# Kernel optimization log

Hardware: AMD Instinct MI355X
Metric: run time of the kernel (lower is better)

## Reference

```python
import jax, jax.numpy as jnp
import numpy as np

B, T, E, H, D_PRICE = 16, 2048, 128, 4, 512


def setup_inputs() -> dict:
    key = jax.random.key(0)
    ks = jax.random.split(key, 22)
    f32 = jnp.float32

    def w(k, shape):
        fan_in = shape[0]
        return (jax.random.normal(k, shape, f32) / np.sqrt(fan_in)).astype(f32)

    def b(k, n):
        return (jax.random.normal(k, (n,), f32) * 0.01).astype(f32)

    inp = {
        # OHLC prices, positive, normalized scale
        "ohlc": jax.random.uniform(ks[0], (B, T, 4), f32, 0.5, 1.5),
        # ohlc_proj: Linear(4, 64)
        "Wp": w(ks[1], (4, 64)), "bp": b(ks[2], 64),
        # curvature_net: Linear(64,128) -> ReLU -> Linear(128,32)
        "Wc1": w(ks[3], (64, 128)), "bc1": b(ks[4], 128),
        "Wc2": w(ks[5], (128, 32)), "bc2": b(ks[6], 32),
        # volatility_net: Linear(64,64) -> ReLU -> Linear(64,16)
        "Wv1": w(ks[7], (64, 64)), "bv1": b(ks[8], 64),
        "Wv2": w(ks[9], (64, 16)), "bv2": b(ks[10], 16),
        # sr_field_net: Linear(64,64) -> ReLU -> Linear(64,16)
        "Ws1": w(ks[11], (64, 64)), "bs1": b(ks[12], 64),
        "Ws2": w(ks[13], (64, 16)), "bs2": b(ks[14], 16),
        # MultiheadAttention(embed_dim=128, num_heads=4): fused in-proj + out-proj
        "Wqkv": w(ks[15], (E, 3 * E)), "bqkv": b(ks[16], 3 * E),
        "Wo": w(ks[17], (E, E)), "bo": b(ks[18], E),
        # output_proj: Linear(128, d_price)
        "Wout": w(ks[19], (E, D_PRICE)), "bout": b(ks[20], D_PRICE),
    }
    return inp


def _mlp(x, W1, b1, W2, b2):
    return jax.nn.relu(x @ W1 + b1) @ W2 + b2


def reference(ohlc, Wp, bp, Wc1, bc1, Wc2, bc2, Wv1, bv1, Wv2, bv2,
              Ws1, bs1, Ws2, bs2, Wqkv, bqkv, Wo, bo, Wout, bout):
    # NB: compute_curvature / compute_volatility_surface / detect_sr_levels
    # in the original forward are dead code (results never used), so they are
    # omitted here; output math is identical.
    e = ohlc @ Wp + bp                                   # [B,T,64]
    feats = jnp.concatenate([
        e,
        _mlp(e, Wc1, bc1, Wc2, bc2),                     # [B,T,32]
        _mlp(e, Wv1, bv1, Wv2, bv2),                     # [B,T,16]
        _mlp(e, Ws1, bs1, Ws2, bs2),                     # [B,T,16]
    ], axis=-1)                                          # [B,T,128]

    Bn, Tn, En = feats.shape
    dh = En // H
    qkv = feats @ Wqkv + bqkv                            # [B,T,3E]
    q, k, v = jnp.split(qkv, 3, axis=-1)

    def heads(x):
        return x.reshape(Bn, Tn, H, dh).transpose(0, 2, 1, 3)  # [B,H,T,dh]

    q, k, v = heads(q), heads(k), heads(v)
    scores = jnp.einsum('bhqd,bhkd->bhqk', q, k) / np.sqrt(dh).astype(feats.dtype)
    a = jax.nn.softmax(scores, axis=-1)                  # [B,H,T,T]
    o = jnp.einsum('bhqk,bhkd->bhqd', a, v)
    o = o.transpose(0, 2, 1, 3).reshape(Bn, Tn, En)
    attended = o @ Wo + bo                               # [B,T,128]

    pooled = attended.mean(axis=1)                       # [B,128]
    return pooled @ Wout + bout                          # [B,512]
```

## Files before the change

### kernel.cpp

```cpp
#include <hip/hip_runtime.h>


typedef __attribute__((ext_vector_type(4)))  float f32x4;
typedef __attribute__((ext_vector_type(16))) float f32x16;
typedef __attribute__((ext_vector_type(4)))  short short4v;
typedef __attribute__((ext_vector_type(8)))  short short8v;

static __device__ __forceinline__ unsigned short f2b(float f) {
    unsigned int u = __builtin_bit_cast(unsigned int, f);
    u += 0x7fffu + ((u >> 16) & 1u);
    return (unsigned short)(u >> 16);
}

static __device__ __forceinline__ unsigned int cvtpk_bf16(float a, float b) {
    unsigned int r;
    asm volatile("v_cvt_pk_bf16_f32 %0, %1, %2" : "=v"(r) : "v"(a), "v"(b));
    return r;
}

__global__ __launch_bounds__(256) void prep_kernel(
    const float* Wc1, const float* Wc2, const float* Wv1, const float* Wv2,
    const float* Ws1, const float* Ws2,
    unsigned short* wc1t, unsigned short* wc2t, unsigned short* wv1t,
    unsigned short* wv2t, unsigned short* ws1t, unsigned short* ws2t,
    float* pooled, float* qkmax)
{
    int idx = blockIdx.x * 256 + threadIdx.x;
    if (idx < 8192)  { int n = idx >> 6, kk = idx & 63;  wc1t[idx] = f2b(Wc1[kk*128 + n]); return; }
    idx -= 8192;
    if (idx < 4096)  { int n = idx >> 7, kk = idx & 127; wc2t[idx] = f2b(Wc2[kk*32  + n]); return; }
    idx -= 4096;
    if (idx < 4096)  { int n = idx >> 6, kk = idx & 63;  wv1t[idx] = f2b(Wv1[kk*64  + n]); return; }
    idx -= 4096;
    if (idx < 1024)  { int n = idx >> 6, kk = idx & 63;  wv2t[idx] = f2b(Wv2[kk*16  + n]); return; }
    idx -= 1024;
    if (idx < 4096)  { int n = idx >> 6, kk = idx & 63;  ws1t[idx] = f2b(Ws1[kk*64  + n]); return; }
    idx -= 4096;
    if (idx < 1024)  { int n = idx >> 6, kk = idx & 63;  ws2t[idx] = f2b(Ws2[kk*16  + n]); return; }
    idx -= 1024;
    if (idx < 2048)  { pooled[idx] = 0.f; return; }
    idx -= 2048;
    if (idx < 128)   qkmax[idx] = 0.f;
}

__global__ __launch_bounds__(256) void wqkv_trans(
    const float* __restrict__ W, unsigned short* __restrict__ outT)
{
    __shared__ float tile[32][33];
    int bidn = blockIdx.x % 12, bidk = blockIdx.x / 12;
    int n0 = bidn * 32, k0 = bidk * 32;
    int tid = threadIdx.x;
    {
        int r = tid >> 3, cq = tid & 7;
        float4 v = *(const float4*)(W + (size_t)(k0 + r) * 384 + n0 + cq * 4);
        tile[r][cq*4+0] = v.x; tile[r][cq*4+1] = v.y;
        tile[r][cq*4+2] = v.z; tile[r][cq*4+3] = v.w;
    }
    __syncthreads();
    {
        int nr = tid >> 3, kq = tid & 7;
        union { unsigned short us[4]; short4v v; } pk;
#pragma unroll
        for (int j = 0; j < 4; ++j) pk.us[j] = f2b(tile[kq*4+j][nr]);
        *(short4v*)(outT + (size_t)(n0 + nr) * 128 + k0 + kq * 4) = pk.v;
    }
}

template<int N, int K, int A_ROWB, bool RELU, bool TO_LDS>
static __device__ __forceinline__ void tile_gemm(
    const char* As, const unsigned short* __restrict__ BT,
    const float* __restrict__ bias, char* Ht,
    unsigned short* __restrict__ gOut, int ocol,
    int m0, int w, int lane)
{
    constexpr int ASL = A_ROWB / 16, NT = N / 16, KS = K / 32;
    int l15 = lane & 15, hi4 = lane >> 4;
    f32x4 acc[NT];
#pragma unroll
    for (int nt = 0; nt < NT; ++nt)
#pragma unroll
        for (int r = 0; r < 4; ++r) acc[nt][r] = 0.f;

#pragma unroll
    for (int ks = 0; ks < KS; ++ks) {
        int slot = ks * 4 + hi4;
        int m = w * 16 + l15;
        short8v af = *(const short8v*)(As + m * A_ROWB + ((slot ^ (m & (ASL - 1))) << 4));
#pragma unroll
        for (int nt = 0; nt < NT; ++nt) {
            int n = nt * 16 + l15;
            short8v bf = *(const short8v*)(BT + (size_t)n * K + slot * 8);
            acc[nt] = __builtin_amdgcn_mfma_f32_16x16x32_bf16(af, bf, acc[nt], 0, 0, 0);
        }
    }
#pragma unroll
    for (int nt = 0; nt < NT; ++nt) {
        int n = nt * 16 + l15;
        float bv = bias[n];
#pragma unroll
        for (int r = 0; r < 4; ++r) {
            int m = w * 16 + hi4 * 4 + r;
            float v = acc[nt][r] + bv;
            if (RELU) v = fmaxf(v, 0.f);
            if (TO_LDS) {
                *(unsigned short*)(Ht + m * 256 + ((((n >> 3) ^ (m & 15))) << 4) + (n & 7) * 2) = f2b(v);
            } else {
                gOut[(size_t)(m0 + m) * 128 + ocol + n] = f2b(v);
            }
        }
    }
}

__global__ __launch_bounds__(256) void fused_mlp(
    const float* __restrict__ ohlc, const float* __restrict__ Wp, const float* __restrict__ bp,
    const unsigned short* __restrict__ wc1t, const float* __restrict__ bc1,
    const unsigned short* __restrict__ wc2t, const float* __restrict__ bc2,
    const unsigned short* __restrict__ wv1t, const float* __restrict__ bv1,
    const unsigned short* __restrict__ wv2t, const float* __restrict__ bv2,
    const unsigned short* __restrict__ ws1t, const float* __restrict__ bs1,
    const unsigned short* __restrict__ ws2t, const float* __restrict__ bs2,
    unsigned short* __restrict__ feats)
{
    __shared__ float wp[256];
    __shared__ float bpl[64];
    __shared__ char Et[64 * 128];
    __shared__ char Ht[64 * 256];

    int tid = threadIdx.x;
    int m0 = blockIdx.x * 64;
    wp[tid] = Wp[tid];
    if (tid < 64) bpl[tid] = bp[tid];
    __syncthreads();

    {
        int tok = tid >> 2, jq = tid & 3;
        float4 ov = ((const float4*)ohlc)[m0 + tok];
#pragma unroll
        for (int c = 0; c < 2; ++c) {
            int sl = jq * 2 + c;
            union { unsigned short us[8]; short8v v; } pk;
#pragma unroll
            for (int jj = 0; jj < 8; ++jj) {
                int j = sl * 8 + jj;
                float e = bpl[j] + ov.x * wp[j] + ov.y * wp[64 + j]
                                 + ov.z * wp[128 + j] + ov.w * wp[192 + j];
                pk.us[jj] = f2b(e);
            }
            *(short8v*)(Et + tok * 128 + ((sl ^ (tok & 7)) << 4)) = pk.v;
            *(short8v*)(feats + (size_t)(m0 + tok) * 128 + sl * 8) = pk.v;
        }
    }
    __syncthreads();

    int lane = tid & 63, w = tid >> 6;
    tile_gemm<128, 64, 128, true,  true >(Et, wc1t, bc1, Ht, feats, 0,   m0, w, lane);
    tile_gemm<32, 128, 256, false, false>(Ht, wc2t, bc2, Ht, feats, 64,  m0, w, lane);
    tile_gemm<64,  64, 128, true,  true >(Et, wv1t, bv1, Ht, feats, 0,   m0, w, lane);
    tile_gemm<16,  64, 256, false, false>(Ht, wv2t, bv2, Ht, feats, 96,  m0, w, lane);
    tile_gemm<64,  64, 128, true,  true >(Et, ws1t, bs1, Ht, feats, 0,   m0, w, lane);
    tile_gemm<16,  64, 256, false, false>(Ht, ws2t, bs2, Ht, feats, 112, m0, w, lane);
}

__global__ __launch_bounds__(256) void qkv_gemm(
    const unsigned short* __restrict__ feats,
    const unsigned short* __restrict__ wqkvt, const float* __restrict__ bqkv,
    unsigned short* __restrict__ qg, unsigned short* __restrict__ kg,
    unsigned short* __restrict__ vTg, float* __restrict__ qkmax)
{
    constexpr int ROWB = 256, CPR = 16;
    __shared__ short8v smemv[4096];
    char* As = (char*)smemv;
    char* Bs = (char*)smemv + 32768;

    int tid = threadIdx.x;
    int m0 = blockIdx.x * 128;
    int sel = blockIdx.y;
    const unsigned short* BT = wqkvt + (size_t)sel * 128 * 128;

    for (int c = tid; c < 128 * CPR; c += 256) {
        int m = c / CPR, s = c % CPR;
        short8v v = *(const short8v*)(feats + (size_t)(m0 + m) * 128 + s * 8);
        *(short8v*)(As + m * ROWB + ((s ^ (m & 15)) * 16)) = v;
    }
    for (int c = tid; c < 128 * CPR; c += 256) {
        int n = c / CPR, s = c % CPR;
        short8v v = *(const short8v*)(BT + (size_t)n * 128 + s * 8);
        *(short8v*)(Bs + n * ROWB + ((s ^ (n & 15)) * 16)) = v;
    }
    __syncthreads();

    int lane = tid & 63, w = tid >> 6;
    int l15 = lane & 15, hi4 = lane >> 4;

    f32x4 acc[2][8];
#pragma unroll
    for (int mt = 0; mt < 2; ++mt)
#pragma unroll
        for (int nt = 0; nt < 8; ++nt)
#pragma unroll
            for (int r = 0; r < 4; ++r) acc[mt][nt][r] = 0.f;

#pragma unroll
    for (int ks = 0; ks < 4; ++ks) {
        int slot = ks * 4 + hi4;
        short8v af[2];
#pragma unroll
        for (int mt = 0; mt < 2; ++mt) {
            int m = w * 32 + mt * 16 + l15;
            af[mt] = *(const short8v*)(As + m * ROWB + ((slot ^ (m & 15)) * 16));
        }
#pragma unroll
        for (int nt = 0; nt < 8; ++nt) {
            int n = nt * 16 + l15;
            short8v bf = *(const short8v*)(Bs + n * ROWB + ((slot ^ (n & 15)) * 16));
            acc[0][nt] = __builtin_amdgcn_mfma_f32_16x16x32_bf16(af[0], bf, acc[0][nt], 0, 0, 0);
            acc[1][nt] = __builtin_amdgcn_mfma_f32_16x16x32_bf16(af[1], bf, acc[1][nt], 0, 0, 0);
        }
    }

    const float QSCALE = 1.4426950408889634f * 0.17677669529663687f;
    int b = m0 >> 11, tp0 = m0 & 2047;

    if (sel == 2) {
#pragma unroll
        for (int mt = 0; mt < 2; ++mt)
#pragma unroll
            for (int nt = 0; nt < 8; ++nt) {
                int n = nt * 16 + l15;
                float bv = bqkv[256 + n];
                int h = n >> 5, dh = n & 31;
                float v0 = acc[mt][nt][0] + bv, v1 = acc[mt][nt][1] + bv;
                float v2 = acc[mt][nt][2] + bv, v3 = acc[mt][nt][3] + bv;
                uint2 pk;
                pk.x = cvtpk_bf16(v0, v1);
                pk.y = cvtpk_bf16(v2, v3);
                int t = tp0 + w * 32 + mt * 16 + hi4 * 4;
                *(uint2*)(vTg + ((size_t)(b * 4 + h) * 32 + dh) * 2048 + t) = pk;
            }
    } else {
        float amax[4] = {0.f, 0.f, 0.f, 0.f};
        float scale = (sel == 0) ? QSCALE : 1.0f;
#pragma unroll
        for (int mt = 0; mt < 2; ++mt)
#pragma unroll
            for (int nt = 0; nt < 8; ++nt) {
                int n = nt * 16 + l15;
                float bv = bqkv[sel * 128 + n];
#pragma unroll
                for (int r = 0; r < 4; ++r) {
                    float v = (acc[mt][nt][r] + bv) * scale;
                    amax[nt >> 1] = fmaxf(amax[nt >> 1], fabsf(v));
                    int m = w * 32 + mt * 16 + hi4 * 4 + r;
                    *(unsigned short*)(As + m * 256 + (((n >> 3) ^ (m & 7)) << 4) + (n & 7) * 2) = f2b(v);
                }
            }
#pragma unroll
        for (int g = 0; g < 4; ++g) {
            float mv = amax[g];
            mv = fmaxf(mv, __shfl_xor(mv, 1));  mv = fmaxf(mv, __shfl_xor(mv, 2));
            mv = fmaxf(mv, __shfl_xor(mv, 4));  mv = fmaxf(mv, __shfl_xor(mv, 8));
            mv = fmaxf(mv, __shfl_xor(mv, 16)); mv = fmaxf(mv, __shfl_xor(mv, 32));
            if (lane == 0)
                atomicMax((int*)(qkmax + sel * 64 + b * 4 + g), __float_as_int(mv));
        }
        __syncthreads();
        unsigned short* og = (sel == 0) ? qg : kg;
#pragma unroll
        for (int it = 0; it < 8; ++it) {
            int ch = it * 256 + tid;
            int m = ch >> 4, c = ch & 15;
            short8v vv = *(const short8v*)(As + m * 256 + ((c ^ (m & 7)) << 4));
            int h = c >> 2, dq = c & 3;
            *(short8v*)(og + ((size_t)(b * 4 + h) * 2048 + tp0 + m) * 32 + dq * 8) = vv;
        }
    }
}

__global__ __launch_bounds__(256) void attn_kernel(
    const unsigned short* __restrict__ qg, const unsigned short* __restrict__ kg,
    const unsigned short* __restrict__ vTg, const float* __restrict__ qkmax,
    float* __restrict__ pooled)
{
    __shared__ short8v VsBuf[4 * 256];
    char* Vs = (char*)VsBuf;

    int tid = threadIdx.x, bid = blockIdx.x;
    int bh = bid & 63, qb = bid >> 6;
    int b = bh >> 2;
    int lane = tid & 63, w = tid >> 6;
    int l31 = lane & 31, hi = lane >> 5;
    int q0 = qb * 128 + w * 32;

    const unsigned short* qrow = qg + ((size_t)bh * 2048 + q0 + l31) * 32;
    short8v Qf0 = *(const short8v*)(qrow + hi * 8);
    short8v Qf1 = *(const short8v*)(qrow + 16 + hi * 8);

    float negM0 = -(32.0f * qkmax[bh] * qkmax[64 + bh]);

    f32x16 accO;
#pragma unroll
    for (int r = 0; r < 16; ++r) accO[r] = 0.f;
    float lsum = 0.f;

    const char* kp = (const char*)(kg + (size_t)bh * 2048 * 32) + (size_t)l31 * 64 + hi * 16;
    int vdh = w * 8 + (lane >> 3);
    const char* vp = (const char*)(vTg + ((size_t)bh * 32 + vdh) * 2048) +
                     (((lane & 7) ^ (vdh & 7)) << 4);
    int vdst = (w * 64 + lane) * 16;

    auto step = [&](int t, short8v (&kC)[4], short8v& vC,
                    short8v (&kN)[4], short8v& vN, char* bufp) {
        if (t < 31) {
            const char* p = kp + (size_t)(t + 1) * 4096;
            kN[0] = *(const short8v*)(p);
            kN[1] = *(const short8v*)(p + 32);
            kN[2] = *(const short8v*)(p + 2048);
            kN[3] = *(const short8v*)(p + 2080);
            vN = *(const short8v*)(vp + (size_t)(t + 1) * 128);
        }
        *(short8v*)(bufp + vdst) = vC;
        asm volatile("s_waitcnt lgkmcnt(0)" ::: "memory");
        __builtin_amdgcn_s_barrier();
        asm volatile("" ::: "memory");
#pragma unroll
        for (int sub = 0; sub < 2; ++sub) {
            f32x16 s;
#pragma unroll
            for (int r = 0; r < 16; ++r) s[r] = negM0;
            s = __builtin_amdgcn_mfma_f32_32x32x16_bf16(kC[sub * 2 + 0], Qf0, s, 0, 0, 0);
            s = __builtin_amdgcn_mfma_f32_32x32x16_bf16(kC[sub * 2 + 1], Qf1, s, 0, 0, 0);
            float p_[16];
            float ps = 0.f;
#pragma unroll
            for (int r = 0; r < 16; ++r) {
                p_[r] = __builtin_amdgcn_exp2f(s[r]);
                ps += p_[r];
            }
            lsum += ps;
#pragma unroll
            for (int c2 = 0; c2 < 2; ++c2) {
                unsigned int wa = cvtpk_bf16(p_[c2 * 8 + 0], p_[c2 * 8 + 1]);
                unsigned int wb = cvtpk_bf16(p_[c2 * 8 + 2], p_[c2 * 8 + 3]);
                unsigned int wc = cvtpk_bf16(p_[c2 * 8 + 4], p_[c2 * 8 + 5]);
                unsigned int wd = cvtpk_bf16(p_[c2 * 8 + 6], p_[c2 * 8 + 7]);
                asm volatile("v_permlane32_swap_b32 %0, %1" : "+v"(wa), "+v"(wc));
                asm volatile("v_permlane32_swap_b32 %0, %1" : "+v"(wb), "+v"(wd));
                union { unsigned int u[4]; short8v v; } pf;
                pf.u[0] = wa; pf.u[1] = wb; pf.u[2] = wc; pf.u[3] = wd;

                short8v vf = *(const short8v*)(bufp + l31 * 128 +
                              (((sub * 4 + c2 * 2 + hi) ^ (l31 & 7)) << 4));
                accO = __builtin_amdgcn_mfma_f32_32x32x16_bf16(vf, pf.v, accO, 0, 0, 0);
            }
        }
    };

    short8v kE[4], kO[4], vE, vO;
    {
        kE[0] = *(const short8v*)(kp);
        kE[1] = *(const short8v*)(kp + 32);
        kE[2] = *(const short8v*)(kp + 2048);
        kE[3] = *(const short8v*)(kp + 2080);
        vE = *(const short8v*)(vp);
    }
#pragma unroll 1
    for (int g = 0; g < 8; ++g) {
        int t0 = g * 4;
        step(t0 + 0, kE, vE, kO, vO, Vs + 0 * 4096);
        step(t0 + 1, kO, vO, kE, vE, Vs + 1 * 4096);
        step(t0 + 2, kE, vE, kO, vO, Vs + 2 * 4096);
        step(t0 + 3, kO, vO, kE, vE, Vs + 3 * 4096);
    }

    lsum += __shfl_xor(lsum, 32);
    float inv = 1.0f / lsum;
#pragma unroll
    for (int r = 0; r < 16; ++r) {
        float v = accO[r] * inv;
        v += __shfl_xor(v, 1); v += __shfl_xor(v, 2); v += __shfl_xor(v, 4);
        v += __shfl_xor(v, 8); v += __shfl_xor(v, 16);
        if (l31 == 0) {
            int dh = (r & 3) + 8 * (r >> 2) + 4 * hi;
            atomicAdd(pooled + b * 128 + (bh & 3) * 32 + dh, v);
        }
    }
}

__global__ __launch_bounds__(256) void head_kernel(
    const float* __restrict__ pooled, const float* __restrict__ Wo,
    const float* __restrict__ bo, const float* __restrict__ Wout,
    const float* __restrict__ bout, float* __restrict__ out)
{
    int bq = blockIdx.x, tid = threadIdx.x;
    __shared__ float pl[128], mid[128];
    if (tid < 128) pl[tid] = pooled[bq * 128 + tid] * (1.f / 2048.f);
    __syncthreads();
    if (tid < 128) {
        float s = bo[tid];
#pragma unroll 4
        for (int c = 0; c < 128; ++c) s += pl[c] * Wo[c * 128 + tid];
        mid[tid] = s;
    }
    __syncthreads();
    for (int j = tid; j < 512; j += 256) {
        float s = bout[j];
#pragma unroll 4
        for (int i = 0; i < 128; ++i) s += mid[i] * Wout[i * 512 + j];
        out[bq * 512 + j] = s;
    }
}

extern "C" void kernel_launch(void* const* d_in, const int* in_sizes, int n_in,
                              void* d_out, int out_size, void* d_ws, size_t ws_size,
                              hipStream_t stream) {
    (void)in_sizes; (void)n_in; (void)out_size; (void)ws_size;
    const float* ohlc = (const float*)d_in[0];
    const float* Wp   = (const float*)d_in[1];  const float* bp   = (const float*)d_in[2];
    const float* Wc1  = (const float*)d_in[3];  const float* bc1  = (const float*)d_in[4];
    const float* Wc2  = (const float*)d_in[5];  const float* bc2  = (const float*)d_in[6];
    const float* Wv1  = (const float*)d_in[7];  const float* bv1  = (const float*)d_in[8];
    const float* Wv2  = (const float*)d_in[9];  const float* bv2  = (const float*)d_in[10];
    const float* Ws1  = (const float*)d_in[11]; const float* bs1  = (const float*)d_in[12];
    const float* Ws2  = (const float*)d_in[13]; const float* bs2  = (const float*)d_in[14];
    const float* Wqkv = (const float*)d_in[15]; const float* bqkv = (const float*)d_in[16];
    const float* Wo   = (const float*)d_in[17]; const float* bo   = (const float*)d_in[18];
    const float* Wout = (const float*)d_in[19]; const float* bout = (const float*)d_in[20];
    float* out = (float*)d_out;
    char* ws = (char*)d_ws;

    const size_t MB8 = 8388608;
    unsigned short* feats = (unsigned short*)(ws);
    unsigned short* qg    = (unsigned short*)(ws + 1 * MB8);
    unsigned short* kg    = (unsigned short*)(ws + 2 * MB8);
    unsigned short* vTg   = (unsigned short*)(ws + 3 * MB8);
    float*          pooled = (float*)(ws + 4 * MB8);
    float*          qkmax  = (float*)(ws + 4 * MB8 + 8192);
    unsigned short* wc1t  = (unsigned short*)(ws + 4 * MB8 + 8192 + 512);
    unsigned short* wc2t  = wc1t + 8192;
    unsigned short* wv1t  = wc2t + 4096;
    unsigned short* wv2t  = wv1t + 4096;
    unsigned short* ws1t  = wv2t + 1024;
    unsigned short* ws2t  = ws1t + 4096;
    unsigned short* wqkvt = ws2t + 1024;

    prep_kernel<<<97, 256, 0, stream>>>(Wc1, Wc2, Wv1, Wv2, Ws1, Ws2,
                                        wc1t, wc2t, wv1t, wv2t, ws1t, ws2t,
                                        pooled, qkmax);
    wqkv_trans<<<48, 256, 0, stream>>>(Wqkv, wqkvt);
    fused_mlp<<<512, 256, 0, stream>>>(ohlc, Wp, bp, wc1t, bc1, wc2t, bc2,
                                       wv1t, bv1, wv2t, bv2, ws1t, bs1, ws2t, bs2, feats);
    qkv_gemm<<<dim3(256, 3), 256, 0, stream>>>(feats, wqkvt, bqkv, qg, kg, vTg, qkmax);
    attn_kernel<<<1024, 256, 0, stream>>>(qg, kg, vTg, qkmax, pooled);
    head_kernel<<<16, 256, 0, stream>>>(pooled, Wo, bo, Wout, bout, out);
}
```

Measured before the change: 155.1 us.

## Fuse MLP and QKV projection into one kernel, compute softmax row sums via MFMA

Merges the MLP feature kernel and the QKV GEMM into a single mega_kernel that keeps the 128-wide feature tile in LDS instead of writing it to global memory and reading it back. The Wqkv transpose is folded into prep_kernel, removing two launches. In attention, the softmax denominator is now accumulated with an extra MFMA against a ones vector rather than scalar adds plus a shuffle, and the score MMA starts from a precomputed NEGM accumulator. s_setprio is raised around the compute phase. The risk is that the fused kernel reads weights per wave from global memory without LDS staging, has smaller M tiles for QKV, and adds MFMA work in the attention inner loop.

```diff
diff --git a/kernel.cpp b/kernel.cpp
--- a/kernel.cpp
+++ b/kernel.cpp
@@ -19,13 +19,34 @@
 }
 
 __global__ __launch_bounds__(256) void prep_kernel(
-    const float* Wc1, const float* Wc2, const float* Wv1, const float* Wv2,
-    const float* Ws1, const float* Ws2,
-    unsigned short* wc1t, unsigned short* wc2t, unsigned short* wv1t,
-    unsigned short* wv2t, unsigned short* ws1t, unsigned short* ws2t,
-    float* pooled, float* qkmax)
-{
-    int idx = blockIdx.x * 256 + threadIdx.x;
+    const float* Wqkv, const float* Wc1, const float* Wc2, const float* Wv1,
+    const float* Wv2, const float* Ws1, const float* Ws2,
+    unsigned short* wqkvt, unsigned short* wc1t, unsigned short* wc2t,
+    unsigned short* wv1t, unsigned short* wv2t, unsigned short* ws1t,
+    unsigned short* ws2t, float* pooled, float* qkmax)
+{
+    int tid = threadIdx.x;
+    if (blockIdx.x < 48) {
+        __shared__ float tile[32][33];
+        int bidn = blockIdx.x % 12, bidk = blockIdx.x / 12;
+        int n0 = bidn * 32, k0 = bidk * 32;
+        {
+            int r = tid >> 3, cq = tid & 7;
+            float4 v = *(const float4*)(Wqkv + (size_t)(k0 + r) * 384 + n0 + cq * 4);
+            tile[r][cq*4+0] = v.x; tile[r][cq*4+1] = v.y;
+            tile[r][cq*4+2] = v.z; tile[r][cq*4+3] = v.w;
+        }
+        __syncthreads();
+        {
+            int nr = tid >> 3, kq = tid & 7;
+            union { unsigned short us[4]; short4v v; } pk;
+#pragma unroll
+            for (int j = 0; j < 4; ++j) pk.us[j] = f2b(tile[kq*4+j][nr]);
+            *(short4v*)(wqkvt + (size_t)(n0 + nr) * 128 + k0 + kq * 4) = pk.v;
+        }
+        return;
+    }
+    int idx = (blockIdx.x - 48) * 256 + tid;
     if (idx < 8192)  { int n = idx >> 6, kk = idx & 63;  wc1t[idx] = f2b(Wc1[kk*128 + n]); return; }
     idx -= 8192;
     if (idx < 4096)  { int n = idx >> 7, kk = idx & 127; wc2t[idx] = f2b(Wc2[kk*32  + n]); return; }
@@ -43,75 +64,91 @@
     if (idx < 128)   qkmax[idx] = 0.f;
 }
 
-__global__ __launch_bounds__(256) void wqkv_trans(
-    const float* __restrict__ W, unsigned short* __restrict__ outT)
-{
-    __shared__ float tile[32][33];
-    int bidn = blockIdx.x % 12, bidk = blockIdx.x / 12;
-    int n0 = bidn * 32, k0 = bidk * 32;
-    int tid = threadIdx.x;
-    {
-        int r = tid >> 3, cq = tid & 7;
-        float4 v = *(const float4*)(W + (size_t)(k0 + r) * 384 + n0 + cq * 4);
-        tile[r][cq*4+0] = v.x; tile[r][cq*4+1] = v.y;
-        tile[r][cq*4+2] = v.z; tile[r][cq*4+3] = v.w;
-    }
-    __syncthreads();
-    {
-        int nr = tid >> 3, kq = tid & 7;
-        union { unsigned short us[4]; short4v v; } pk;
-#pragma unroll
-        for (int j = 0; j < 4; ++j) pk.us[j] = f2b(tile[kq*4+j][nr]);
-        *(short4v*)(outT + (size_t)(n0 + nr) * 128 + k0 + kq * 4) = pk.v;
-    }
-}
-
-template<int N, int K, int A_ROWB, bool RELU, bool TO_LDS>
-static __device__ __forceinline__ void tile_gemm(
+template<int N, int K>
+static __device__ __forceinline__ void wave_gemm(
     const char* As, const unsigned short* __restrict__ BT,
-    const float* __restrict__ bias, char* Ht,
-    unsigned short* __restrict__ gOut, int ocol,
-    int m0, int w, int lane)
-{
-    constexpr int ASL = A_ROWB / 16, NT = N / 16, KS = K / 32;
+    int w, int lane, f32x4 (&acc)[N / 16])
+{
     int l15 = lane & 15, hi4 = lane >> 4;
-    f32x4 acc[NT];
-#pragma unroll
-    for (int nt = 0; nt < NT; ++nt)
+#pragma unroll
+    for (int nt = 0; nt < N / 16; ++nt)
 #pragma unroll
         for (int r = 0; r < 4; ++r) acc[nt][r] = 0.f;
-
-#pragma unroll
-    for (int ks = 0; ks < KS; ++ks) {
+#pragma unroll
+    for (int ks = 0; ks < K / 32; ++ks) {
         int slot = ks * 4 + hi4;
         int m = w * 16 + l15;
-        short8v af = *(const short8v*)(As + m * A_ROWB + ((slot ^ (m & (ASL - 1))) << 4));
-#pragma unroll
-        for (int nt = 0; nt < NT; ++nt) {
+        short8v af = *(const short8v*)(As + m * 256 + ((slot ^ (m & 15)) << 4));
+#pragma unroll
+        for (int nt = 0; nt < N / 16; ++nt) {
             int n = nt * 16 + l15;
             short8v bf = *(const short8v*)(BT + (size_t)n * K + slot * 8);
             acc[nt] = __builtin_amdgcn_mfma_f32_16x16x32_bf16(af, bf, acc[nt], 0, 0, 0);
         }
     }
-#pragma unroll
-    for (int nt = 0; nt < NT; ++nt) {
+}
+
+template<int N, bool RELU>
+static __device__ __forceinline__ void epi_lds(
+    f32x4 (&acc)[N / 16], const float* __restrict__ bias, int boff,
+    char* dst, int ocol, int w, int lane)
+{
+    int l15 = lane & 15, hi4 = lane >> 4;
+#pragma unroll
+    for (int nt = 0; nt < N / 16; ++nt) {
         int n = nt * 16 + l15;
-        float bv = bias[n];
+        float bv = bias[boff + n];
 #pragma unroll
         for (int r = 0; r < 4; ++r) {
             int m = w * 16 + hi4 * 4 + r;
             float v = acc[nt][r] + bv;
             if (RELU) v = fmaxf(v, 0.f);
-            if (TO_LDS) {
-                *(unsigned short*)(Ht + m * 256 + ((((n >> 3) ^ (m & 15))) << 4) + (n & 7) * 2) = f2b(v);
-            } else {
-                gOut[(size_t)(m0 + m) * 128 + ocol + n] = f2b(v);
-            }
-        }
-    }
-}
-
-__global__ __launch_bounds__(256) void fused_mlp(
+            int col = ocol + n;
+            *(unsigned short*)(dst + m * 256 + (((col >> 3) ^ (m & 15)) << 4) + (col & 7) * 2) = f2b(v);
+        }
+    }
+}
+
+static __device__ __forceinline__ void epi_qk(
+    f32x4 (&acc)[8], const float* __restrict__ bias, int boff, float scale,
+    unsigned short* __restrict__ og, float* qkmaxp,
+    int b, int tp0, int w, int lane, char* bounce)
+{
+    int l15 = lane & 15, hi4 = lane >> 4;
+    float amax[4] = {0.f, 0.f, 0.f, 0.f};
+#pragma unroll
+    for (int nt = 0; nt < 8; ++nt) {
+        int n = nt * 16 + l15;
+        float bv = bias[boff + n];
+#pragma unroll
+        for (int r = 0; r < 4; ++r) {
+            int m = w * 16 + hi4 * 4 + r;
+            float v = (acc[nt][r] + bv) * scale;
+            amax[nt >> 1] = fmaxf(amax[nt >> 1], fabsf(v));
+            *(unsigned short*)(bounce + m * 256 + (((n >> 3) ^ (m & 15)) << 4) + (n & 7) * 2) = f2b(v);
+        }
+    }
+#pragma unroll
+    for (int g = 0; g < 4; ++g) {
+        float mv = amax[g];
+        mv = fmaxf(mv, __shfl_xor(mv, 1));  mv = fmaxf(mv, __shfl_xor(mv, 2));
+        mv = fmaxf(mv, __shfl_xor(mv, 4));  mv = fmaxf(mv, __shfl_xor(mv, 8));
+        mv = fmaxf(mv, __shfl_xor(mv, 16)); mv = fmaxf(mv, __shfl_xor(mv, 32));
+        if (lane == 0)
+            atomicMax((int*)(qkmaxp + b * 4 + g), __float_as_int(mv));
+    }
+#pragma unroll
+    for (int it = 0; it < 4; ++it) {
+        int ch = it * 64 + lane;
+        int ml = ch >> 4, c = ch & 15;
+        int m = w * 16 + ml;
+        short8v vv = *(const short8v*)(bounce + m * 256 + ((c ^ (m & 15)) << 4));
+        int h = c >> 2, dq = c & 3;
+        *(short8v*)(og + ((size_t)(b * 4 + h) * 2048 + tp0 + m) * 32 + dq * 8) = vv;
+    }
+}
+
+__global__ __launch_bounds__(256) void mega_kernel(
     const float* __restrict__ ohlc, const float* __restrict__ Wp, const float* __restrict__ bp,
     const unsigned short* __restrict__ wc1t, const float* __restrict__ bc1,
     const unsigned short* __restrict__ wc2t, const float* __restrict__ bc2,
@@ -119,11 +156,13 @@
     const unsigned short* __restrict__ wv2t, const float* __restrict__ bv2,
     const unsigned short* __restrict__ ws1t, const float* __restrict__ bs1,
     const unsigned short* __restrict__ ws2t, const float* __restrict__ bs2,
-    unsigned short* __restrict__ feats)
+    const unsigned short* __restrict__ wqkvt, const float* __restrict__ bqkv,
+    unsigned short* __restrict__ qg, unsigned short* __restrict__ kg,
+    unsigned short* __restrict__ vTg, float* __restrict__ qkmax)
 {
     __shared__ float wp[256];
     __shared__ float bpl[64];
-    __shared__ char Et[64 * 128];
+    __shared__ char Ft[64 * 256];
     __shared__ char Ht[64 * 256];
 
     int tid = threadIdx.x;
@@ -146,132 +185,68 @@
                                  + ov.z * wp[128 + j] + ov.w * wp[192 + j];
                 pk.us[jj] = f2b(e);
             }
-            *(short8v*)(Et + tok * 128 + ((sl ^ (tok & 7)) << 4)) = pk.v;
-            *(short8v*)(feats + (size_t)(m0 + tok) * 128 + sl * 8) = pk.v;
-        }
-    }
-    __syncthreads();
+            *(short8v*)(Ft + tok * 256 + ((sl ^ (tok & 15)) << 4)) = pk.v;
+        }
+    }
 
     int lane = tid & 63, w = tid >> 6;
-    tile_gemm<128, 64, 128, true,  true >(Et, wc1t, bc1, Ht, feats, 0,   m0, w, lane);
-    tile_gemm<32, 128, 256, false, false>(Ht, wc2t, bc2, Ht, feats, 64,  m0, w, lane);
-    tile_gemm<64,  64, 128, true,  true >(Et, wv1t, bv1, Ht, feats, 0,   m0, w, lane);
-    tile_gemm<16,  64, 256, false, false>(Ht, wv2t, bv2, Ht, feats, 96,  m0, w, lane);
-    tile_gemm<64,  64, 128, true,  true >(Et, ws1t, bs1, Ht, feats, 0,   m0, w, lane);
-    tile_gemm<16,  64, 256, false, false>(Ht, ws2t, bs2, Ht, feats, 112, m0, w, lane);
-}
-
-__global__ __launch_bounds__(256) void qkv_gemm(
-    const unsigned short* __restrict__ feats,
-    const unsigned short* __restrict__ wqkvt, const float* __restrict__ bqkv,
-    unsigned short* __restrict__ qg, unsigned short* __restrict__ kg,
-    unsigned short* __restrict__ vTg, float* __restrict__ qkmax)
-{
-    constexpr int ROWB = 256, CPR = 16;
-    __shared__ short8v smemv[4096];
-    char* As = (char*)smemv;
-    char* Bs = (char*)smemv + 32768;
-
-    int tid = threadIdx.x;
-    int m0 = blockIdx.x * 128;
-    int sel = blockIdx.y;
-    const unsigned short* BT = wqkvt + (size_t)sel * 128 * 128;
-
-    for (int c = tid; c < 128 * CPR; c += 256) {
-        int m = c / CPR, s = c % CPR;
-        short8v v = *(const short8v*)(feats + (size_t)(m0 + m) * 128 + s * 8);
-        *(short8v*)(As + m * ROWB + ((s ^ (m & 15)) * 16)) = v;
-    }
-    for (int c = tid; c < 128 * CPR; c += 256) {
-        int n = c / CPR, s = c % CPR;
-        short8v v = *(const short8v*)(BT + (size_t)n * 128 + s * 8);
-        *(short8v*)(Bs + n * ROWB + ((s ^ (n & 15)) * 16)) = v;
-    }
-    __syncthreads();
-
-    int lane = tid & 63, w = tid >> 6;
-    int l15 = lane & 15, hi4 = lane >> 4;
-
-    f32x4 acc[2][8];
-#pragma unroll
-    for (int mt = 0; mt < 2; ++mt)
-#pragma unroll
-        for (int nt = 0; nt < 8; ++nt)
-#pragma unroll
-            for (int r = 0; r < 4; ++r) acc[mt][nt][r] = 0.f;
-
-#pragma unroll
-    for (int ks = 0; ks < 4; ++ks) {
-        int slot = ks * 4 + hi4;
-        short8v af[2];
-#pragma unroll
-        for (int mt = 0; mt < 2; ++mt) {
-            int m = w * 32 + mt * 16 + l15;
-            af[mt] = *(const short8v*)(As + m * ROWB + ((slot ^ (m & 15)) * 16));
-        }
+    {
+        f32x4 a8[8];
+        wave_gemm<128, 64>(Ft, wc1t, w, lane, a8);
+        epi_lds<128, true>(a8, bc1, 0, Ht, 0, w, lane);
+    }
+    {
+        f32x4 a2[2];
+        wave_gemm<32, 128>(Ht, wc2t, w, lane, a2);
+        epi_lds<32, false>(a2, bc2, 0, Ft, 64, w, lane);
+    }
+    {
+        f32x4 a4[4];
+        wave_gemm<64, 64>(Ft, wv1t, w, lane, a4);
+        epi_lds<64, true>(a4, bv1, 0, Ht, 0, w, lane);
+    }
+    {
+        f32x4 a1[1];
+        wave_gemm<16, 64>(Ht, wv2t, w, lane, a1);
+        epi_lds<16, false>(a1, bv2, 0, Ft, 96, w, lane);
+    }
+    {
+        f32x4 a4[4];
+        wave_gemm<64, 64>(Ft, ws1t, w, lane, a4);
+        epi_lds<64, true>(a4, bs1, 0, Ht, 0, w, lane);
+    }
+    {
+        f32x4 a1[1];
+        wave_gemm<16, 64>(Ht, ws2t, w, lane, a1);
+        epi_lds<16, false>(a1, bs2, 0, Ft, 112, w, lane);
+    }
+
+    const float QSCALE = 1.4426950408889634f * 0.17677669529663687f;
+    int b = m0 >> 11, tp0 = m0 & 2047;
+    {
+        f32x4 aq[8];
+        wave_gemm<128, 128>(Ft, wqkvt, w, lane, aq);
+        epi_qk(aq, bqkv, 0, QSCALE, qg, qkmax, b, tp0, w, lane, Ht);
+    }
+    {
+        f32x4 ak[8];
+        wave_gemm<128, 128>(Ft, wqkvt + 128 * 128, w, lane, ak);
+        epi_qk(ak, bqkv, 128, 1.0f, kg, qkmax + 64, b, tp0, w, lane, Ht);
+    }
+    {
+        f32x4 av[8];
+        wave_gemm<128, 128>(Ft, wqkvt + 2 * 128 * 128, w, lane, av);
+        int l15 = lane & 15, hi4 = lane >> 4;
 #pragma unroll
         for (int nt = 0; nt < 8; ++nt) {
             int n = nt * 16 + l15;
-            short8v bf = *(const short8v*)(Bs + n * ROWB + ((slot ^ (n & 15)) * 16));
-            acc[0][nt] = __builtin_amdgcn_mfma_f32_16x16x32_bf16(af[0], bf, acc[0][nt], 0, 0, 0);
-            acc[1][nt] = __builtin_amdgcn_mfma_f32_16x16x32_bf16(af[1], bf, acc[1][nt], 0, 0, 0);
-        }
-    }
-
-    const float QSCALE = 1.4426950408889634f * 0.17677669529663687f;
-    int b = m0 >> 11, tp0 = m0 & 2047;
-
-    if (sel == 2) {
-#pragma unroll
-        for (int mt = 0; mt < 2; ++mt)
-#pragma unroll
-            for (int nt = 0; nt < 8; ++nt) {
-                int n = nt * 16 + l15;
-                float bv = bqkv[256 + n];
-                int h = n >> 5, dh = n & 31;
-                float v0 = acc[mt][nt][0] + bv, v1 = acc[mt][nt][1] + bv;
-                float v2 = acc[mt][nt][2] + bv, v3 = acc[mt][nt][3] + bv;
-                uint2 pk;
-                pk.x = cvtpk_bf16(v0, v1);
-                pk.y = cvtpk_bf16(v2, v3);
-                int t = tp0 + w * 32 + mt * 16 + hi4 * 4;
-                *(uint2*)(vTg + ((size_t)(b * 4 + h) * 32 + dh) * 2048 + t) = pk;
-            }
-    } else {
-        float amax[4] = {0.f, 0.f, 0.f, 0.f};
-        float scale = (sel == 0) ? QSCALE : 1.0f;
-#pragma unroll
-        for (int mt = 0; mt < 2; ++mt)
-#pragma unroll
-            for (int nt = 0; nt < 8; ++nt) {
-                int n = nt * 16 + l15;
-                float bv = bqkv[sel * 128 + n];
-#pragma unroll
-                for (int r = 0; r < 4; ++r) {
-                    float v = (acc[mt][nt][r] + bv) * scale;
-                    amax[nt >> 1] = fmaxf(amax[nt >> 1], fabsf(v));
-                    int m = w * 32 + mt * 16 + hi4 * 4 + r;
-                    *(unsigned short*)(As + m * 256 + (((n >> 3) ^ (m & 7)) << 4) + (n & 7) * 2) = f2b(v);
-                }
-            }
-#pragma unroll
-        for (int g = 0; g < 4; ++g) {
-            float mv = amax[g];
-            mv = fmaxf(mv, __shfl_xor(mv, 1));  mv = fmaxf(mv, __shfl_xor(mv, 2));
-            mv = fmaxf(mv, __shfl_xor(mv, 4));  mv = fmaxf(mv, __shfl_xor(mv, 8));
-            mv = fmaxf(mv, __shfl_xor(mv, 16)); mv = fmaxf(mv, __shfl_xor(mv, 32));
-            if (lane == 0)
-                atomicMax((int*)(qkmax + sel * 64 + b * 4 + g), __float_as_int(mv));
-        }
-        __syncthreads();
-        unsigned short* og = (sel == 0) ? qg : kg;
-#pragma unroll
-        for (int it = 0; it < 8; ++it) {
-            int ch = it * 256 + tid;
-            int m = ch >> 4, c = ch & 15;
-            short8v vv = *(const short8v*)(As + m * 256 + ((c ^ (m & 7)) << 4));
-            int h = c >> 2, dq = c & 3;
-            *(short8v*)(og + ((size_t)(b * 4 + h) * 2048 + tp0 + m) * 32 + dq * 8) = vv;
+            float bv = bqkv[256 + n];
+            int h = n >> 5, dh = n & 31;
+            uint2 pk;
+            pk.x = cvtpk_bf16(av[nt][0] + bv, av[nt][1] + bv);
+            pk.y = cvtpk_bf16(av[nt][2] + bv, av[nt][3] + bv);
+            int t = tp0 + w * 16 + hi4 * 4;
+            *(uint2*)(vTg + ((size_t)(b * 4 + h) * 32 + dh) * 2048 + t) = pk;
         }
     }
 }
@@ -296,17 +271,31 @@
     short8v Qf1 = *(const short8v*)(qrow + 16 + hi * 8);
 
     float negM0 = -(32.0f * qkmax[bh] * qkmax[64 + bh]);
-
-    f32x16 accO;
-#pragma unroll
-    for (int r = 0; r < 16; ++r) accO[r] = 0.f;
-    float lsum = 0.f;
+    f32x16 NEGM;
+#pragma unroll
+    for (int r = 0; r < 16; ++r) NEGM[r] = negM0;
+
+    f32x16 accO, lacc;
+#pragma unroll
+    for (int r = 0; r < 16; ++r) { accO[r] = 0.f; lacc[r] = 0.f; }
+
+    short8v ONES;
+    {
+        union { unsigned short us[8]; short8v v; } u;
+#pragma unroll
+        for (int j = 0; j < 8; ++j) u.us[j] = 0x3F80;
+        ONES = u.v;
+    }
 
     const char* kp = (const char*)(kg + (size_t)bh * 2048 * 32) + (size_t)l31 * 64 + hi * 16;
     int vdh = w * 8 + (lane >> 3);
     const char* vp = (const char*)(vTg + ((size_t)bh * 32 + vdh) * 2048) +
                      (((lane & 7) ^ (vdh & 7)) << 4);
     int vdst = (w * 64 + lane) * 16;
+    int voff[4];
+#pragma unroll
+    for (int j = 0; j < 4; ++j)
+        voff[j] = l31 * 128 + (((2 * j + hi) ^ (l31 & 7)) << 4);
 
     auto step = [&](int t, short8v (&kC)[4], short8v& vC,
                     short8v (&kN)[4], short8v& vN, char* bufp) {
@@ -322,21 +311,14 @@
         asm volatile("s_waitcnt lgkmcnt(0)" ::: "memory");
         __builtin_amdgcn_s_barrier();
         asm volatile("" ::: "memory");
+        __builtin_amdgcn_s_setprio(1);
 #pragma unroll
         for (int sub = 0; sub < 2; ++sub) {
-            f32x16 s;
-#pragma unroll
-            for (int r = 0; r < 16; ++r) s[r] = negM0;
-            s = __builtin_amdgcn_mfma_f32_32x32x16_bf16(kC[sub * 2 + 0], Qf0, s, 0, 0, 0);
+            f32x16 s = __builtin_amdgcn_mfma_f32_32x32x16_bf16(kC[sub * 2 + 0], Qf0, NEGM, 0, 0, 0);
             s = __builtin_amdgcn_mfma_f32_32x32x16_bf16(kC[sub * 2 + 1], Qf1, s, 0, 0, 0);
             float p_[16];
-            float ps = 0.f;
-#pragma unroll
-            for (int r = 0; r < 16; ++r) {
-                p_[r] = __builtin_amdgcn_exp2f(s[r]);
-                ps += p_[r];
-            }
-            lsum += ps;
+#pragma unroll
+            for (int r = 0; r < 16; ++r) p_[r] = __builtin_amdgcn_exp2f(s[r]);
 #pragma unroll
             for (int c2 = 0; c2 < 2; ++c2) {
                 unsigned int wa = cvtpk_bf16(p_[c2 * 8 + 0], p_[c2 * 8 + 1]);
@@ -348,11 +330,12 @@
                 union { unsigned int u[4]; short8v v; } pf;
                 pf.u[0] = wa; pf.u[1] = wb; pf.u[2] = wc; pf.u[3] = wd;
 
-                short8v vf = *(const short8v*)(bufp + l31 * 128 +
-                              (((sub * 4 + c2 * 2 + hi) ^ (l31 & 7)) << 4));
+                lacc = __builtin_amdgcn_mfma_f32_32x32x16_bf16(ONES, pf.v, lacc, 0, 0, 0);
+                short8v vf = *(const short8v*)(bufp + voff[sub * 2 + c2]);
                 accO = __builtin_amdgcn_mfma_f32_32x32x16_bf16(vf, pf.v, accO, 0, 0, 0);
             }
         }
+        __builtin_amdgcn_s_setprio(0);
     };
 
     short8v kE[4], kO[4], vE, vO;
@@ -372,8 +355,7 @@
         step(t0 + 3, kO, vO, kE, vE, Vs + 3 * 4096);
     }
 
-    lsum += __shfl_xor(lsum, 32);
-    float inv = 1.0f / lsum;
+    float inv = 1.0f / (lacc[0] + 1e-30f);
 #pragma unroll
     for (int r = 0; r < 16; ++r) {
         float v = accO[r] * inv;
@@ -429,13 +411,12 @@
     char* ws = (char*)d_ws;
 
     const size_t MB8 = 8388608;
-    unsigned short* feats = (unsigned short*)(ws);
-    unsigned short* qg    = (unsigned short*)(ws + 1 * MB8);
-    unsigned short* kg    = (unsigned short*)(ws + 2 * MB8);
-    unsigned short* vTg   = (unsigned short*)(ws + 3 * MB8);
-    float*          pooled = (float*)(ws + 4 * MB8);
-    float*          qkmax  = (float*)(ws + 4 * MB8 + 8192);
-    unsigned short* wc1t  = (unsigned short*)(ws + 4 * MB8 + 8192 + 512);
+    unsigned short* qg    = (unsigned short*)(ws);
+    unsigned short* kg    = (unsigned short*)(ws + 1 * MB8);
+    unsigned short* vTg   = (unsigned short*)(ws + 2 * MB8);
+    float*          pooled = (float*)(ws + 3 * MB8);
+    float*          qkmax  = (float*)(ws + 3 * MB8 + 8192);
+    unsigned short* wc1t  = (unsigned short*)(ws + 3 * MB8 + 8192 + 512);
     unsigned short* wc2t  = wc1t + 8192;
     unsigned short* wv1t  = wc2t + 4096;
     unsigned short* wv2t  = wv1t + 4096;
@@ -443,13 +424,12 @@
     unsigned short* ws2t  = ws1t + 4096;
     unsigned short* wqkvt = ws2t + 1024;
 
-    prep_kernel<<<97, 256, 0, stream>>>(Wc1, Wc2, Wv1, Wv2, Ws1, Ws2,
-                                        wc1t, wc2t, wv1t, wv2t, ws1t, ws2t,
-                                        pooled, qkmax);
-    wqkv_trans<<<48, 256, 0, stream>>>(Wqkv, wqkvt);
-    fused_mlp<<<512, 256, 0, stream>>>(ohlc, Wp, bp, wc1t, bc1, wc2t, bc2,
-                                       wv1t, bv1, wv2t, bv2, ws1t, bs1, ws2t, bs2, feats);
-    qkv_gemm<<<dim3(256, 3), 256, 0, stream>>>(feats, wqkvt, bqkv, qg, kg, vTg, qkmax);
+    prep_kernel<<<145, 256, 0, stream>>>(Wqkv, Wc1, Wc2, Wv1, Wv2, Ws1, Ws2,
+                                         wqkvt, wc1t, wc2t, wv1t, wv2t, ws1t, ws2t,
+                                         pooled, qkmax);
+    mega_kernel<<<512, 256, 0, stream>>>(ohlc, Wp, bp, wc1t, bc1, wc2t, bc2,
+                                         wv1t, bv1, wv2t, bv2, ws1t, bs1, ws2t, bs2,
+                                         wqkvt, bqkv, qg, kg, vTg, qkmax);
     attn_kernel<<<1024, 256, 0, stream>>>(qg, kg, vTg, qkmax, pooled);
     head_kernel<<<16, 256, 0, stream>>>(pooled, Wo, bo, Wout, bout, out);
 }
```

After: 181.4 us. +17.0%, slower.

## Drop LDS staging of V in attention, compute row sums via MFMA, merge prep kernels

Applied to the files above, without the earlier changes.

The attention kernel now loads V fragments directly from global memory into registers per lane instead of staging them through a shared-memory ring buffer with a block barrier each step. The softmax denominator is accumulated with an extra MFMA against a ones vector rather than scalar adds plus a cross-lane shuffle. The Wqkv transpose is folded into the prep kernel, removing one launch. This removes per-step barriers and LDS traffic, at the cost of each wave re-reading V from global/L2 (four times the V loads per lane) and one extra MFMA per PV MFMA.

```diff
diff --git a/kernel.cpp b/kernel.cpp
--- a/kernel.cpp
+++ b/kernel.cpp
@@ -19,13 +19,34 @@
 }
 
 __global__ __launch_bounds__(256) void prep_kernel(
-    const float* Wc1, const float* Wc2, const float* Wv1, const float* Wv2,
-    const float* Ws1, const float* Ws2,
-    unsigned short* wc1t, unsigned short* wc2t, unsigned short* wv1t,
-    unsigned short* wv2t, unsigned short* ws1t, unsigned short* ws2t,
-    float* pooled, float* qkmax)
-{
-    int idx = blockIdx.x * 256 + threadIdx.x;
+    const float* Wqkv, const float* Wc1, const float* Wc2, const float* Wv1,
+    const float* Wv2, const float* Ws1, const float* Ws2,
+    unsigned short* wqkvt, unsigned short* wc1t, unsigned short* wc2t,
+    unsigned short* wv1t, unsigned short* wv2t, unsigned short* ws1t,
+    unsigned short* ws2t, float* pooled, float* qkmax)
+{
+    int tid = threadIdx.x;
+    if (blockIdx.x < 48) {
+        __shared__ float tile[32][33];
+        int bidn = blockIdx.x % 12, bidk = blockIdx.x / 12;
+        int n0 = bidn * 32, k0 = bidk * 32;
+        {
+            int r = tid >> 3, cq = tid & 7;
+            float4 v = *(const float4*)(Wqkv + (size_t)(k0 + r) * 384 + n0 + cq * 4);
+            tile[r][cq*4+0] = v.x; tile[r][cq*4+1] = v.y;
+            tile[r][cq*4+2] = v.z; tile[r][cq*4+3] = v.w;
+        }
+        __syncthreads();
+        {
+            int nr = tid >> 3, kq = tid & 7;
+            union { unsigned short us[4]; short4v v; } pk;
+#pragma unroll
+            for (int j = 0; j < 4; ++j) pk.us[j] = f2b(tile[kq*4+j][nr]);
+            *(short4v*)(wqkvt + (size_t)(n0 + nr) * 128 + k0 + kq * 4) = pk.v;
+        }
+        return;
+    }
+    int idx = (blockIdx.x - 48) * 256 + tid;
     if (idx < 8192)  { int n = idx >> 6, kk = idx & 63;  wc1t[idx] = f2b(Wc1[kk*128 + n]); return; }
     idx -= 8192;
     if (idx < 4096)  { int n = idx >> 7, kk = idx & 127; wc2t[idx] = f2b(Wc2[kk*32  + n]); return; }
@@ -43,29 +64,6 @@
     if (idx < 128)   qkmax[idx] = 0.f;
 }
 
-__global__ __launch_bounds__(256) void wqkv_trans(
-    const float* __restrict__ W, unsigned short* __restrict__ outT)
-{
-    __shared__ float tile[32][33];
-    int bidn = blockIdx.x % 12, bidk = blockIdx.x / 12;
-    int n0 = bidn * 32, k0 = bidk * 32;
-    int tid = threadIdx.x;
-    {
-        int r = tid >> 3, cq = tid & 7;
-        float4 v = *(const float4*)(W + (size_t)(k0 + r) * 384 + n0 + cq * 4);
-        tile[r][cq*4+0] = v.x; tile[r][cq*4+1] = v.y;
-        tile[r][cq*4+2] = v.z; tile[r][cq*4+3] = v.w;
-    }
-    __syncthreads();
-    {
-        int nr = tid >> 3, kq = tid & 7;
-        union { unsigned short us[4]; short4v v; } pk;
-#pragma unroll
-        for (int j = 0; j < 4; ++j) pk.us[j] = f2b(tile[kq*4+j][nr]);
-        *(short4v*)(outT + (size_t)(n0 + nr) * 128 + k0 + kq * 4) = pk.v;
-    }
-}
-
 template<int N, int K, int A_ROWB, bool RELU, bool TO_LDS>
 static __device__ __forceinline__ void tile_gemm(
     const char* As, const unsigned short* __restrict__ BT,
@@ -281,9 +279,6 @@
     const unsigned short* __restrict__ vTg, const float* __restrict__ qkmax,
     float* __restrict__ pooled)
 {
-    __shared__ short8v VsBuf[4 * 256];
-    char* Vs = (char*)VsBuf;
-
     int tid = threadIdx.x, bid = blockIdx.x;
     int bh = bid & 63, qb = bid >> 6;
     int b = bh >> 2;
@@ -296,47 +291,48 @@
     short8v Qf1 = *(const short8v*)(qrow + 16 + hi * 8);
 
     float negM0 = -(32.0f * qkmax[bh] * qkmax[64 + bh]);
-
-    f32x16 accO;
-#pragma unroll
-    for (int r = 0; r < 16; ++r) accO[r] = 0.f;
-    float lsum = 0.f;
-
-    const char* kp = (const char*)(kg + (size_t)bh * 2048 * 32) + (size_t)l31 * 64 + hi * 16;
-    int vdh = w * 8 + (lane >> 3);
-    const char* vp = (const char*)(vTg + ((size_t)bh * 32 + vdh) * 2048) +
-                     (((lane & 7) ^ (vdh & 7)) << 4);
-    int vdst = (w * 64 + lane) * 16;
-
-    auto step = [&](int t, short8v (&kC)[4], short8v& vC,
-                    short8v (&kN)[4], short8v& vN, char* bufp) {
+    f32x16 NEGM;
+#pragma unroll
+    for (int r = 0; r < 16; ++r) NEGM[r] = negM0;
+
+    f32x16 accO, lacc;
+#pragma unroll
+    for (int r = 0; r < 16; ++r) { accO[r] = 0.f; lacc[r] = 0.f; }
+
+    short8v ONES;
+    {
+        union { unsigned short us[8]; short8v v; } u;
+#pragma unroll
+        for (int j = 0; j < 8; ++j) u.us[j] = 0x3F80;
+        ONES = u.v;
+    }
+
+    const char* kb = (const char*)kg + (size_t)bh * 131072 + l31 * 64 + hi * 16;
+    const char* vb = (const char*)vTg + ((size_t)bh * 32 + l31) * 4096 + hi * 16;
+
+    auto step = [&](int t, short8v (&kC)[4], short8v (&kN)[4]) {
+        short8v vC[4];
+        {
+            const char* p = vb + (size_t)t * 128;
+            vC[0] = *(const short8v*)(p);
+            vC[1] = *(const short8v*)(p + 32);
+            vC[2] = *(const short8v*)(p + 64);
+            vC[3] = *(const short8v*)(p + 96);
+        }
         if (t < 31) {
-            const char* p = kp + (size_t)(t + 1) * 4096;
+            const char* p = kb + (size_t)(t + 1) * 4096;
             kN[0] = *(const short8v*)(p);
             kN[1] = *(const short8v*)(p + 32);
             kN[2] = *(const short8v*)(p + 2048);
             kN[3] = *(const short8v*)(p + 2080);
-            vN = *(const short8v*)(vp + (size_t)(t + 1) * 128);
-        }
-        *(short8v*)(bufp + vdst) = vC;
-        asm volatile("s_waitcnt lgkmcnt(0)" ::: "memory");
-        __builtin_amdgcn_s_barrier();
-        asm volatile("" ::: "memory");
+        }
 #pragma unroll
         for (int sub = 0; sub < 2; ++sub) {
-            f32x16 s;
-#pragma unroll
-            for (int r = 0; r < 16; ++r) s[r] = negM0;
-            s = __builtin_amdgcn_mfma_f32_32x32x16_bf16(kC[sub * 2 + 0], Qf0, s, 0, 0, 0);
+            f32x16 s = __builtin_amdgcn_mfma_f32_32x32x16_bf16(kC[sub * 2 + 0], Qf0, NEGM, 0, 0, 0);
             s = __builtin_amdgcn_mfma_f32_32x32x16_bf16(kC[sub * 2 + 1], Qf1, s, 0, 0, 0);
             float p_[16];
-            float ps = 0.f;
-#pragma unroll
-            for (int r = 0; r < 16; ++r) {
-                p_[r] = __builtin_amdgcn_exp2f(s[r]);
-                ps += p_[r];
-            }
-            lsum += ps;
+#pragma unroll
+            for (int r = 0; r < 16; ++r) p_[r] = __builtin_amdgcn_exp2f(s[r]);
 #pragma unroll
             for (int c2 = 0; c2 < 2; ++c2) {
                 unsigned int wa = cvtpk_bf16(p_[c2 * 8 + 0], p_[c2 * 8 + 1]);
@@ -348,32 +344,26 @@
                 union { unsigned int u[4]; short8v v; } pf;
                 pf.u[0] = wa; pf.u[1] = wb; pf.u[2] = wc; pf.u[3] = wd;
 
-                short8v vf = *(const short8v*)(bufp + l31 * 128 +
-                              (((sub * 4 + c2 * 2 + hi) ^ (l31 & 7)) << 4));
-                accO = __builtin_amdgcn_mfma_f32_32x32x16_bf16(vf, pf.v, accO, 0, 0, 0);
+                lacc = __builtin_amdgcn_mfma_f32_32x32x16_bf16(ONES, pf.v, lacc, 0, 0, 0);
+                accO = __builtin_amdgcn_mfma_f32_32x32x16_bf16(vC[sub * 2 + c2], pf.v, accO, 0, 0, 0);
             }
         }
     };
 
-    short8v kE[4], kO[4], vE, vO;
+    short8v kE[4], kO[4];
     {
-        kE[0] = *(const short8v*)(kp);
-        kE[1] = *(const short8v*)(kp + 32);
-        kE[2] = *(const short8v*)(kp + 2048);
-        kE[3] = *(const short8v*)(kp + 2080);
-        vE = *(const short8v*)(vp);
+        kE[0] = *(const short8v*)(kb);
+        kE[1] = *(const short8v*)(kb + 32);
+        kE[2] = *(const short8v*)(kb + 2048);
+        kE[3] = *(const short8v*)(kb + 2080);
     }
 #pragma unroll 1
-    for (int g = 0; g < 8; ++g) {
-        int t0 = g * 4;
-        step(t0 + 0, kE, vE, kO, vO, Vs + 0 * 4096);
-        step(t0 + 1, kO, vO, kE, vE, Vs + 1 * 4096);
-        step(t0 + 2, kE, vE, kO, vO, Vs + 2 * 4096);
-        step(t0 + 3, kO, vO, kE, vE, Vs + 3 * 4096);
-    }
-
-    lsum += __shfl_xor(lsum, 32);
-    float inv = 1.0f / lsum;
+    for (int g = 0; g < 16; ++g) {
+        step(2 * g, kE, kO);
+        step(2 * g + 1, kO, kE);
+    }
+
+    float inv = 1.0f / (lacc[0] + 1e-30f);
 #pragma unroll
     for (int r = 0; r < 16; ++r) {
         float v = accO[r] * inv;
@@ -443,10 +433,9 @@
     unsigned short* ws2t  = ws1t + 4096;
     unsigned short* wqkvt = ws2t + 1024;
 
-    prep_kernel<<<97, 256, 0, stream>>>(Wc1, Wc2, Wv1, Wv2, Ws1, Ws2,
-                                        wc1t, wc2t, wv1t, wv2t, ws1t, ws2t,
-                                        pooled, qkmax);
-    wqkv_trans<<<48, 256, 0, stream>>>(Wqkv, wqkvt);
+    prep_kernel<<<145, 256, 0, stream>>>(Wqkv, Wc1, Wc2, Wv1, Wv2, Ws1, Ws2,
+                                         wqkvt, wc1t, wc2t, wv1t, wv2t, ws1t, ws2t,
+                                         pooled, qkmax);
     fused_mlp<<<512, 256, 0, stream>>>(ohlc, Wp, bp, wc1t, bc1, wc2t, bc2,
                                        wv1t, bv1, wv2t, bv2, ws1t, bs1, ws2t, bs2, feats);
     qkv_gemm<<<dim3(256, 3), 256, 0, stream>>>(feats, wqkvt, bqkv, qg, kg, vTg, qkmax);
```

After: 185.9 us. 1.2x slower.
